# Kernel optimization log

Hardware: AMD Instinct MI355X
Metric: run time of the kernel (lower is better)

## Reference

```python
import jax, jax.numpy as jnp
import numpy as np

S, B, H = 2048, 32, 1024


def setup_inputs() -> dict:
    key = jax.random.key(0)
    k1, k2, k3, k4 = jax.random.split(key, 4)
    hidden = jax.random.normal(k1, (B, H), dtype=jnp.float32)
    encoder_outputs = jax.random.normal(k2, (S, B, H), dtype=jnp.float32)
    # nn.Linear(H, H): weight [H, H] (applied as x @ W^T), bias [H]
    W = jax.random.normal(k3, (H, H), dtype=jnp.float32) / np.sqrt(H)
    b = jax.random.normal(k4, (H,), dtype=jnp.float32) / np.sqrt(H)
    return {"hidden": hidden, "encoder_outputs": encoder_outputs, "W": W, "b": b}


def reference(hidden, encoder_outputs, W, b):
    # energy[s,b,:] = Linear(encoder_outputs[s,b,:]) = enc @ W^T + b
    energy = jnp.einsum('sbh,kh->sbk', encoder_outputs, W) + b  # [S,B,H]
    # score[b,s] = hidden[b] . energy[s,b]  (the diag-of-matmul in the loop)
    attn_energies = jnp.einsum('bh,sbh->bs', hidden, energy)  # [B,S]
    after_softmax = jax.nn.softmax(attn_energies, axis=1)      # softmax over seq_len
    return after_softmax[None, :, :]  # [1,B,S]
```

## Files before the change

### kernel.cpp

```cpp
#include <hip/hip_runtime.h>

#define SEQ 2048
#define BATCH 32
#define HID 1024

__global__ void __launch_bounds__(256) vproj_kernel(const float* __restrict__ hidden,
                                                    const float* __restrict__ W,
                                                    float* __restrict__ v) {
    const int b = blockIdx.x;
    const int t = threadIdx.x;
    __shared__ float sh[HID];
    for (int i = t; i < HID; i += 256) sh[i] = hidden[b * HID + i];
    __syncthreads();

    const float4* __restrict__ W4 = (const float4*)W;
    float4 acc = make_float4(0.f, 0.f, 0.f, 0.f);
#pragma unroll 8
    for (int k = 0; k < HID; ++k) {
        const float hk = sh[k];
        const float4 w = W4[k * (HID / 4) + t];
        acc.x = fmaf(hk, w.x, acc.x);
        acc.y = fmaf(hk, w.y, acc.y);
        acc.z = fmaf(hk, w.z, acc.z);
        acc.w = fmaf(hk, w.w, acc.w);
    }
    ((float4*)v)[b * (HID / 4) + t] = acc;
}

__global__ void __launch_bounds__(256) score_kernel(const float* __restrict__ enc,
                                                    const float* __restrict__ v,
                                                    float* __restrict__ scores) {
    const int s = blockIdx.x;
    const int wave = threadIdx.x >> 6;
    const int lane = threadIdx.x & 63;
    const int b = blockIdx.y * 4 + wave;

    const float4* __restrict__ e4 = (const float4*)(enc + ((size_t)s * BATCH + b) * HID);
    const float4* __restrict__ v4 = (const float4*)(v + b * HID);

    float acc = 0.f;
#pragma unroll
    for (int j = 0; j < 4; ++j) {
        const float4 e = e4[j * 64 + lane];
        const float4 w = v4[j * 64 + lane];
        acc = fmaf(e.x, w.x, acc);
        acc = fmaf(e.y, w.y, acc);
        acc = fmaf(e.z, w.z, acc);
        acc = fmaf(e.w, w.w, acc);
    }
#pragma unroll
    for (int off = 32; off > 0; off >>= 1) acc += __shfl_xor(acc, off, 64);
    if (lane == 0) scores[b * SEQ + s] = acc;
}

__global__ void __launch_bounds__(256) softmax_kernel(const float* __restrict__ scores,
                                                      float* __restrict__ out) {
    const int b = blockIdx.x;
    const int t = threadIdx.x;
    __shared__ float red[256];

    float x[8];
    float m = -INFINITY;
#pragma unroll
    for (int j = 0; j < 8; ++j) {
        x[j] = scores[b * SEQ + t + j * 256];
        m = fmaxf(m, x[j]);
    }
    red[t] = m;
    __syncthreads();
    for (int o = 128; o > 0; o >>= 1) {
        if (t < o) red[t] = fmaxf(red[t], red[t + o]);
        __syncthreads();
    }
    m = red[0];
    __syncthreads();

    float sum = 0.f;
#pragma unroll
    for (int j = 0; j < 8; ++j) {
        x[j] = __expf(x[j] - m);
        sum += x[j];
    }
    red[t] = sum;
    __syncthreads();
    for (int o = 128; o > 0; o >>= 1) {
        if (t < o) red[t] += red[t + o];
        __syncthreads();
    }
    const float inv = 1.f / red[0];
#pragma unroll
    for (int j = 0; j < 8; ++j) out[b * SEQ + t + j * 256] = x[j] * inv;
}

extern "C" void kernel_launch(void* const* d_in, const int* in_sizes, int n_in,
                              void* d_out, int out_size, void* d_ws, size_t ws_size,
                              hipStream_t stream) {
    const float* hidden = (const float*)d_in[0];
    const float* enc    = (const float*)d_in[1];
    const float* W      = (const float*)d_in[2];
    float* out = (float*)d_out;

    float* v      = (float*)d_ws;
    float* scores = v + BATCH * HID;

    vproj_kernel<<<BATCH, 256, 0, stream>>>(hidden, W, v);
    score_kernel<<<dim3(SEQ, BATCH / 4), 256, 0, stream>>>(enc, v, scores);
    softmax_kernel<<<BATCH, 256, 0, stream>>>(scores, out);
}
```

Measured before the change: 443.1 us.

## Split vproj GEMV over output chunks and K-slices with shared-memory reduction

The hidden-by-W projection grid grows from 32 blocks to 32x8 blocks. Each block handles 128 output columns, and each group of 32 threads within it covers a 128-long slice of the reduction dimension. Partial sums are then combined through a shared-memory tree. This is meant to fix the low occupancy and long serial load chain of the original kernel, which used only 32 workgroups. In exchange it adds extra barriers and a shared-memory reduction.

```diff
diff --git a/kernel.cpp b/kernel.cpp
--- a/kernel.cpp
+++ b/kernel.cpp
@@ -7,24 +7,50 @@
 __global__ void __launch_bounds__(256) vproj_kernel(const float* __restrict__ hidden,
                                                     const float* __restrict__ W,
                                                     float* __restrict__ v) {
-    const int b = blockIdx.x;
-    const int t = threadIdx.x;
-    __shared__ float sh[HID];
-    for (int i = t; i < HID; i += 256) sh[i] = hidden[b * HID + i];
+    const int b  = blockIdx.x;
+    const int hc = blockIdx.y;
+    const int t  = threadIdx.x;
+    const int h4 = hc * 32 + (t & 31);
+    const int kk = t >> 5;
+
+    __shared__ float  sh[HID];
+    __shared__ float4 red[256];
+
+    ((float4*)sh)[t] = ((const float4*)(hidden + b * HID))[t];
     __syncthreads();
 
     const float4* __restrict__ W4 = (const float4*)W;
     float4 acc = make_float4(0.f, 0.f, 0.f, 0.f);
+    const int k0 = kk * 128;
 #pragma unroll 8
-    for (int k = 0; k < HID; ++k) {
-        const float hk = sh[k];
-        const float4 w = W4[k * (HID / 4) + t];
+    for (int k = k0; k < k0 + 128; ++k) {
+        const float  hk = sh[k];
+        const float4 w  = W4[k * (HID / 4) + h4];
         acc.x = fmaf(hk, w.x, acc.x);
         acc.y = fmaf(hk, w.y, acc.y);
         acc.z = fmaf(hk, w.z, acc.z);
         acc.w = fmaf(hk, w.w, acc.w);
     }
-    ((float4*)v)[b * (HID / 4) + t] = acc;
+
+    red[t] = acc;
+    __syncthreads();
+    if (t < 128) {
+        float4 a = red[t], c = red[t + 128];
+        a.x += c.x; a.y += c.y; a.z += c.z; a.w += c.w;
+        red[t] = a;
+    }
+    __syncthreads();
+    if (t < 64) {
+        float4 a = red[t], c = red[t + 64];
+        a.x += c.x; a.y += c.y; a.z += c.z; a.w += c.w;
+        red[t] = a;
+    }
+    __syncthreads();
+    if (t < 32) {
+        float4 a = red[t], c = red[t + 32];
+        a.x += c.x; a.y += c.y; a.z += c.z; a.w += c.w;
+        ((float4*)v)[b * (HID / 4) + hc * 32 + t] = a;
+    }
 }
 
 __global__ void __launch_bounds__(256) score_kernel(const float* __restrict__ enc,
@@ -103,7 +129,7 @@
     float* v      = (float*)d_ws;
     float* scores = v + BATCH * HID;
 
-    vproj_kernel<<<BATCH, 256, 0, stream>>>(hidden, W, v);
+    vproj_kernel<<<dim3(BATCH, 8), 256, 0, stream>>>(hidden, W, v);
     score_kernel<<<dim3(SEQ, BATCH / 4), 256, 0, stream>>>(enc, v, scores);
     softmax_kernel<<<BATCH, 256, 0, stream>>>(scores, out);
 }
```

Result: faster. 377.9 us (-14.7%).
